# Kernel optimization log

Measured on AMD Instinct MI355X. Metric: run time of the kernel, lower is better.

Reference implementation:

```python
import jax, jax.numpy as jnp
import numpy as np


def setup_inputs() -> dict:
    key = jax.random.key(0)
    k1, k2, k3 = jax.random.split(key, 3)
    N, D, E = 16384, 4096, 64
    x = jax.random.normal(k1, (N, D), dtype=jnp.float32)
    W = jax.random.normal(k2, (E, D), dtype=jnp.float32) * (1.0 / np.sqrt(D))
    b = jax.random.normal(k3, (E,), dtype=jnp.float32) * 0.01
    return {"x": x, "W": W, "b": b, "top_k": 2}


def reference(x, W, b, top_k):
    # logits: [N, E]
    logits = jnp.einsum('nd,ed->ne', x, W) + b
    top_vals, top_idx = jax.lax.top_k(logits, top_k)          # [N, k]
    top_probs = jax.nn.softmax(top_vals, axis=-1)             # softmax over the k selected logits
    N = logits.shape[0]
    rows = jnp.arange(N)[:, None]                             # [N, 1]
    gates = jnp.zeros_like(logits).at[rows, top_idx].set(top_probs)  # sparse gate tensor [N, E]
    return gates, top_idx
```

## Files before the change

### kernel.cpp

```cpp
#include <hip/hip_runtime.h>
#include <math.h>

typedef _Float16 f16;
typedef _Float16 f16x8 __attribute__((ext_vector_type(8)));
typedef _Float16 f16x4 __attribute__((ext_vector_type(4)));
typedef float    f32x4 __attribute__((ext_vector_type(4)));

constexpr int D_DIM = 4096;
constexpr int E_DIM = 64;
constexpr int BM    = 64;
constexpr int BK    = 64;
constexpr int NT    = 256;
constexpr int LDT   = BK + 8;
constexpr int LDL   = E_DIM + 1;

constexpr float XSCALE  = 8.0f;
constexpr float WSCALE  = 256.0f;
constexpr float UNSCALE = 1.0f / 2048.0f;

__global__ __launch_bounds__(NT) void pack_w(const float* __restrict__ W,
                                             f16* __restrict__ whi,
                                             f16* __restrict__ wlo) {
    const int i = (blockIdx.x * NT + threadIdx.x) * 4;
    const float4 w = *(const float4*)(W + i);
    const float v[4] = {w.x * WSCALE, w.y * WSCALE, w.z * WSCALE, w.w * WSCALE};
    f16x4 hv, lv;
#pragma unroll
    for (int j = 0; j < 4; ++j) {
        const f16 h = (f16)v[j];
        hv[j] = h;
        lv[j] = (f16)(v[j] - (float)h);
    }
    *(f16x4*)(whi + i) = hv;
    *(f16x4*)(wlo + i) = lv;
}

__global__ __launch_bounds__(NT, 4) void gemm_partial(
    const float* __restrict__ x, const f16* __restrict__ whi,
    const f16* __restrict__ wlo, float* __restrict__ partials, int ksplit)
{
    __shared__ alignas(16) f16 Wh[E_DIM * LDT];
    __shared__ alignas(16) f16 Wl[E_DIM * LDT];

    const int tid   = threadIdx.x;
    const int bx    = blockIdx.x;
    const int tile  = bx / ksplit;
    const int split = bx % ksplit;
    const int row0  = tile * BM;
    const int dk    = D_DIM / ksplit;
    const int koff  = split * dk;
    const int KT    = dk / BK;

    const int ks2 = tid & 3;
    const int we  = tid >> 2;

    const int lane = tid & 63;
    const int wv   = tid >> 6;
    const int r0   = wv * 16;
    const int m    = lane & 15;
    const int quad = lane >> 4;

    f32x4 acc[4] = {{0,0,0,0},{0,0,0,0},{0,0,0,0},{0,0,0,0}};

    f16x8 whr[2], wlr[2];
    auto loadW = [&](int t) {
        const size_t o = (size_t)we * D_DIM + koff + t * BK + ks2 * 16;
        whr[0] = *(const f16x8*)(whi + o);
        whr[1] = *(const f16x8*)(whi + o + 8);
        wlr[0] = *(const f16x8*)(wlo + o);
        wlr[1] = *(const f16x8*)(wlo + o + 8);
    };
    auto storeW = [&]() {
        *(f16x8*)&Wh[we * LDT + ks2 * 16]     = whr[0];
        *(f16x8*)&Wh[we * LDT + ks2 * 16 + 8] = whr[1];
        *(f16x8*)&Wl[we * LDT + ks2 * 16]     = wlr[0];
        *(f16x8*)&Wl[we * LDT + ks2 * 16 + 8] = wlr[1];
    };

    const float* xrow = x + (size_t)(row0 + r0 + m) * D_DIM + koff + quad * 8;

    float4 xc[2][2], xn[2][2];
    auto loadX = [&](float4 d[2][2], int t) {
#pragma unroll
        for (int kk = 0; kk < 2; ++kk) {
            const float* p = xrow + t * BK + kk * 32;
            d[kk][0] = ((const float4*)p)[0];
            d[kk][1] = ((const float4*)p)[1];
        }
    };

    loadW(0);
    loadX(xc, 0);
    storeW();
    __syncthreads();

    for (int t = 0; t < KT; ++t) {
        if (t + 1 < KT) { loadW(t + 1); loadX(xn, t + 1); }

#pragma unroll
        for (int kk = 0; kk < 2; ++kk) {
            const float v[8] = {xc[kk][0].x * XSCALE, xc[kk][0].y * XSCALE,
                                xc[kk][0].z * XSCALE, xc[kk][0].w * XSCALE,
                                xc[kk][1].x * XSCALE, xc[kk][1].y * XSCALE,
                                xc[kk][1].z * XSCALE, xc[kk][1].w * XSCALE};
            f16x8 ah, al;
#pragma unroll
            for (int j = 0; j < 8; ++j) {
                const f16 h = (f16)v[j];
                ah[j] = h;
                al[j] = (f16)(v[j] - (float)h);
            }
            const int ko = kk * 32 + quad * 8;
#pragma unroll
            for (int ct = 0; ct < 4; ++ct) {
                const f16x8 bh = *(const f16x8*)&Wh[(ct * 16 + m) * LDT + ko];
                const f16x8 bl = *(const f16x8*)&Wl[(ct * 16 + m) * LDT + ko];
                acc[ct] = __builtin_amdgcn_mfma_f32_16x16x32_f16(ah, bh, acc[ct], 0, 0, 0);
                acc[ct] = __builtin_amdgcn_mfma_f32_16x16x32_f16(al, bh, acc[ct], 0, 0, 0);
                acc[ct] = __builtin_amdgcn_mfma_f32_16x16x32_f16(ah, bl, acc[ct], 0, 0, 0);
            }
        }
        __syncthreads();
        if (t + 1 < KT) {
            storeW();
#pragma unroll
            for (int kk = 0; kk < 2; ++kk) { xc[kk][0] = xn[kk][0]; xc[kk][1] = xn[kk][1]; }
        }
        __syncthreads();
    }

    float* my = partials + (size_t)bx * (BM * E_DIM);
#pragma unroll
    for (int ct = 0; ct < 4; ++ct)
#pragma unroll
        for (int reg = 0; reg < 4; ++reg)
            my[(r0 + quad * 4 + reg) * E_DIM + ct * 16 + m] = acc[ct][reg] * UNSCALE;
}

__global__ __launch_bounds__(NT) void topk_finish_kernel(
    const float* __restrict__ partials, const float* __restrict__ b,
    float* __restrict__ out, int ksplit, int N)
{
    __shared__ float smem[BM * LDL + 256];
    float* Ls  = smem;
    float* aux = smem + BM * LDL;

    const int tid  = threadIdx.x;
    const int tile = blockIdx.x;
    const int row0 = tile * BM;
    const float* base = partials + (size_t)tile * ksplit * (BM * E_DIM);

#pragma unroll
    for (int p = 0; p < 4; ++p) {
        const int f4 = p * 256 + tid;
        const int r  = f4 >> 4;
        const int c4 = f4 & 15;
        float4 s = *(const float4*)(base + (size_t)f4 * 4);
        for (int sp = 1; sp < ksplit; ++sp) {
            const float4 t4 = *(const float4*)(base + (size_t)sp * (BM * E_DIM) + (size_t)f4 * 4);
            s.x += t4.x; s.y += t4.y; s.z += t4.z; s.w += t4.w;
        }
        const float4 bb = ((const float4*)b)[c4];
        Ls[r * LDL + c4 * 4 + 0] = s.x + bb.x;
        Ls[r * LDL + c4 * 4 + 1] = s.y + bb.y;
        Ls[r * LDL + c4 * 4 + 2] = s.z + bb.z;
        Ls[r * LDL + c4 * 4 + 3] = s.w + bb.w;
    }
    __syncthreads();

    if (tid < BM) {
        const float* lr = &Ls[tid * LDL];
        float v1 = -INFINITY, v2 = -INFINITY;
        int i1 = 0, i2 = 0;
        for (int e = 0; e < E_DIM; ++e) {
            const float v = lr[e];
            if (v > v1)      { v2 = v1; i2 = i1; v1 = v; i1 = e; }
            else if (v > v2) { v2 = v;  i2 = e; }
        }
        const float ex = expf(v2 - v1);
        const float dn = 1.0f + ex;
        aux[tid]       = (float)i1;
        aux[64 + tid]  = (float)i2;
        aux[128 + tid] = 1.0f / dn;
        aux[192 + tid] = ex / dn;
        const size_t basei = (size_t)N * E_DIM + (size_t)(row0 + tid) * 2;
        out[basei]     = (float)i1;
        out[basei + 1] = (float)i2;
    }
    __syncthreads();

#pragma unroll
    for (int p = 0; p < 4; ++p) {
        const int f4 = p * 256 + tid;
        const int r  = f4 >> 4;
        const int c4 = f4 & 15;
        const int i1 = (int)aux[r];
        const int i2 = (int)aux[64 + r];
        const float p1 = aux[128 + r];
        const float p2 = aux[192 + r];
        const int e = c4 * 4;
        float4 g;
        g.x = (e + 0 == i1) ? p1 : (e + 0 == i2) ? p2 : 0.0f;
        g.y = (e + 1 == i1) ? p1 : (e + 1 == i2) ? p2 : 0.0f;
        g.z = (e + 2 == i1) ? p1 : (e + 2 == i2) ? p2 : 0.0f;
        g.w = (e + 3 == i1) ? p1 : (e + 3 == i2) ? p2 : 0.0f;
        *(float4*)(out + (size_t)(row0 + r) * E_DIM + e) = g;
    }
}

extern "C" void kernel_launch(void* const* d_in, const int* in_sizes, int n_in,
                              void* d_out, int out_size, void* d_ws, size_t ws_size,
                              hipStream_t stream) {
    const float* x = (const float*)d_in[0];
    const float* W = (const float*)d_in[1];
    const float* b = (const float*)d_in[2];
    float* out = (float*)d_out;
    const int N = in_sizes[0] / D_DIM;
    const int ntiles = N / BM;

    f16* whi = (f16*)d_ws;
    f16* wlo = whi + (size_t)E_DIM * D_DIM;
    float* partials = (float*)(wlo + (size_t)E_DIM * D_DIM);

    const size_t wplanes = 2 * (size_t)E_DIM * D_DIM * sizeof(f16);
    const size_t pbytes  = (size_t)BM * E_DIM * sizeof(float);
    int ksplit = 1;
    if      (ws_size >= wplanes + (size_t)ntiles * 4 * pbytes) ksplit = 4;
    else if (ws_size >= wplanes + (size_t)ntiles * 2 * pbytes) ksplit = 2;

    hipLaunchKernelGGL(pack_w, dim3((E_DIM * D_DIM) / (NT * 4)), dim3(NT),
                       0, stream, W, whi, wlo);
    hipLaunchKernelGGL(gemm_partial, dim3(ntiles * ksplit), dim3(NT),
                       0, stream, x, whi, wlo, partials, ksplit);
    hipLaunchKernelGGL(topk_finish_kernel, dim3(ntiles), dim3(NT),
                       0, stream, partials, b, out, ksplit, N);
}
```

Measured before the change: 392.1 us.

## Fuse gating GEMM with top-k finish using in-block K split

Merges the partial GEMM and the top-k/softmax finish kernel into one kernel. Each block now handles 32 rows, and its four waves split the K dimension into two halves, which are reduced through shared memory before the top-k. This removes the global partials buffer round trip and one kernel launch. The cost is that each block now stages both W halves into shared memory, raising LDS use and halving the rows that share each W tile load, so W traffic per row doubles.

```diff
diff --git a/kernel.cpp b/kernel.cpp
--- a/kernel.cpp
+++ b/kernel.cpp
@@ -6,13 +6,16 @@
 typedef _Float16 f16x4 __attribute__((ext_vector_type(4)));
 typedef float    f32x4 __attribute__((ext_vector_type(4)));
 
-constexpr int D_DIM = 4096;
-constexpr int E_DIM = 64;
-constexpr int BM    = 64;
-constexpr int BK    = 64;
-constexpr int NT    = 256;
-constexpr int LDT   = BK + 8;
-constexpr int LDL   = E_DIM + 1;
+constexpr int D_DIM   = 4096;
+constexpr int E_DIM   = 64;
+constexpr int BM      = 32;
+constexpr int BK      = 64;
+constexpr int NT      = 256;
+constexpr int KHALVES = 2;
+constexpr int DK      = D_DIM / KHALVES;
+constexpr int KT      = DK / BK;
+constexpr int LDT     = BK + 8;
+constexpr int LDL     = E_DIM + 1;
 
 constexpr float XSCALE  = 8.0f;
 constexpr float WSCALE  = 256.0f;
@@ -35,46 +38,52 @@
     *(f16x4*)(wlo + i) = lv;
 }
 
-__global__ __launch_bounds__(NT, 4) void gemm_partial(
+__global__ __launch_bounds__(NT, 2) void moe_gate_fused(
     const float* __restrict__ x, const f16* __restrict__ whi,
-    const f16* __restrict__ wlo, float* __restrict__ partials, int ksplit)
+    const f16* __restrict__ wlo, const float* __restrict__ b,
+    float* __restrict__ out, int N)
 {
-    __shared__ alignas(16) f16 Wh[E_DIM * LDT];
-    __shared__ alignas(16) f16 Wl[E_DIM * LDT];
-
-    const int tid   = threadIdx.x;
-    const int bx    = blockIdx.x;
-    const int tile  = bx / ksplit;
-    const int split = bx % ksplit;
-    const int row0  = tile * BM;
-    const int dk    = D_DIM / ksplit;
-    const int koff  = split * dk;
-    const int KT    = dk / BK;
+    __shared__ alignas(16) f16 Wh[KHALVES][E_DIM * LDT];
+    __shared__ alignas(16) f16 Wl[KHALVES][E_DIM * LDT];
+    __shared__ float Ls[BM * LDL];
+    __shared__ float aux[4 * BM];
+
+    const int tid  = threadIdx.x;
+    const int row0 = blockIdx.x * BM;
 
     const int ks2 = tid & 3;
     const int we  = tid >> 2;
 
     const int lane = tid & 63;
     const int wv   = tid >> 6;
-    const int r0   = wv * 16;
+    const int half = wv >> 1;
+    const int rg   = wv & 1;
+    const int r0   = rg * 16;
     const int m    = lane & 15;
     const int quad = lane >> 4;
+    const int koff = half * DK;
 
     f32x4 acc[4] = {{0,0,0,0},{0,0,0,0},{0,0,0,0},{0,0,0,0}};
 
-    f16x8 whr[2], wlr[2];
+    f16x8 whr[KHALVES][2], wlr[KHALVES][2];
     auto loadW = [&](int t) {
-        const size_t o = (size_t)we * D_DIM + koff + t * BK + ks2 * 16;
-        whr[0] = *(const f16x8*)(whi + o);
-        whr[1] = *(const f16x8*)(whi + o + 8);
-        wlr[0] = *(const f16x8*)(wlo + o);
-        wlr[1] = *(const f16x8*)(wlo + o + 8);
+#pragma unroll
+        for (int h = 0; h < KHALVES; ++h) {
+            const size_t o = (size_t)we * D_DIM + h * DK + t * BK + ks2 * 16;
+            whr[h][0] = *(const f16x8*)(whi + o);
+            whr[h][1] = *(const f16x8*)(whi + o + 8);
+            wlr[h][0] = *(const f16x8*)(wlo + o);
+            wlr[h][1] = *(const f16x8*)(wlo + o + 8);
+        }
     };
     auto storeW = [&]() {
-        *(f16x8*)&Wh[we * LDT + ks2 * 16]     = whr[0];
-        *(f16x8*)&Wh[we * LDT + ks2 * 16 + 8] = whr[1];
-        *(f16x8*)&Wl[we * LDT + ks2 * 16]     = wlr[0];
-        *(f16x8*)&Wl[we * LDT + ks2 * 16 + 8] = wlr[1];
+#pragma unroll
+        for (int h = 0; h < KHALVES; ++h) {
+            *(f16x8*)&Wh[h][we * LDT + ks2 * 16]     = whr[h][0];
+            *(f16x8*)&Wh[h][we * LDT + ks2 * 16 + 8] = whr[h][1];
+            *(f16x8*)&Wl[h][we * LDT + ks2 * 16]     = wlr[h][0];
+            *(f16x8*)&Wl[h][we * LDT + ks2 * 16 + 8] = wlr[h][1];
+        }
     };
 
     const float* xrow = x + (size_t)(row0 + r0 + m) * D_DIM + koff + quad * 8;
@@ -113,8 +122,8 @@
             const int ko = kk * 32 + quad * 8;
 #pragma unroll
             for (int ct = 0; ct < 4; ++ct) {
-                const f16x8 bh = *(const f16x8*)&Wh[(ct * 16 + m) * LDT + ko];
-                const f16x8 bl = *(const f16x8*)&Wl[(ct * 16 + m) * LDT + ko];
+                const f16x8 bh = *(const f16x8*)&Wh[half][(ct * 16 + m) * LDT + ko];
+                const f16x8 bl = *(const f16x8*)&Wl[half][(ct * 16 + m) * LDT + ko];
                 acc[ct] = __builtin_amdgcn_mfma_f32_16x16x32_f16(ah, bh, acc[ct], 0, 0, 0);
                 acc[ct] = __builtin_amdgcn_mfma_f32_16x16x32_f16(al, bh, acc[ct], 0, 0, 0);
                 acc[ct] = __builtin_amdgcn_mfma_f32_16x16x32_f16(ah, bl, acc[ct], 0, 0, 0);
@@ -129,42 +138,23 @@
         __syncthreads();
     }
 
-    float* my = partials + (size_t)bx * (BM * E_DIM);
-#pragma unroll
-    for (int ct = 0; ct < 4; ++ct)
-#pragma unroll
-        for (int reg = 0; reg < 4; ++reg)
-            my[(r0 + quad * 4 + reg) * E_DIM + ct * 16 + m] = acc[ct][reg] * UNSCALE;
-}
-
-__global__ __launch_bounds__(NT) void topk_finish_kernel(
-    const float* __restrict__ partials, const float* __restrict__ b,
-    float* __restrict__ out, int ksplit, int N)
-{
-    __shared__ float smem[BM * LDL + 256];
-    float* Ls  = smem;
-    float* aux = smem + BM * LDL;
-
-    const int tid  = threadIdx.x;
-    const int tile = blockIdx.x;
-    const int row0 = tile * BM;
-    const float* base = partials + (size_t)tile * ksplit * (BM * E_DIM);
-
-#pragma unroll
-    for (int p = 0; p < 4; ++p) {
-        const int f4 = p * 256 + tid;
-        const int r  = f4 >> 4;
-        const int c4 = f4 & 15;
-        float4 s = *(const float4*)(base + (size_t)f4 * 4);
-        for (int sp = 1; sp < ksplit; ++sp) {
-            const float4 t4 = *(const float4*)(base + (size_t)sp * (BM * E_DIM) + (size_t)f4 * 4);
-            s.x += t4.x; s.y += t4.y; s.z += t4.z; s.w += t4.w;
-        }
-        const float4 bb = ((const float4*)b)[c4];
-        Ls[r * LDL + c4 * 4 + 0] = s.x + bb.x;
-        Ls[r * LDL + c4 * 4 + 1] = s.y + bb.y;
-        Ls[r * LDL + c4 * 4 + 2] = s.z + bb.z;
-        Ls[r * LDL + c4 * 4 + 3] = s.w + bb.w;
+    if (half == 1) {
+#pragma unroll
+        for (int ct = 0; ct < 4; ++ct)
+#pragma unroll
+            for (int reg = 0; reg < 4; ++reg)
+                Ls[(r0 + quad * 4 + reg) * LDL + ct * 16 + m] = acc[ct][reg];
+    }
+    __syncthreads();
+    if (half == 0) {
+#pragma unroll
+        for (int ct = 0; ct < 4; ++ct)
+#pragma unroll
+            for (int reg = 0; reg < 4; ++reg) {
+                const int r = r0 + quad * 4 + reg;
+                const int e = ct * 16 + m;
+                Ls[r * LDL + e] = (acc[ct][reg] + Ls[r * LDL + e]) * UNSCALE + b[e];
+            }
     }
     __syncthreads();
 
@@ -179,10 +169,10 @@
         }
         const float ex = expf(v2 - v1);
         const float dn = 1.0f + ex;
-        aux[tid]       = (float)i1;
-        aux[64 + tid]  = (float)i2;
-        aux[128 + tid] = 1.0f / dn;
-        aux[192 + tid] = ex / dn;
+        aux[tid]          = (float)i1;
+        aux[BM + tid]     = (float)i2;
+        aux[2 * BM + tid] = 1.0f / dn;
+        aux[3 * BM + tid] = ex / dn;
         const size_t basei = (size_t)N * E_DIM + (size_t)(row0 + tid) * 2;
         out[basei]     = (float)i1;
         out[basei + 1] = (float)i2;
@@ -190,14 +180,14 @@
     __syncthreads();
 
 #pragma unroll
-    for (int p = 0; p < 4; ++p) {
-        const int f4 = p * 256 + tid;
+    for (int p = 0; p < 2; ++p) {
+        const int f4 = p * NT + tid;
         const int r  = f4 >> 4;
         const int c4 = f4 & 15;
         const int i1 = (int)aux[r];
-        const int i2 = (int)aux[64 + r];
-        const float p1 = aux[128 + r];
-        const float p2 = aux[192 + r];
+        const int i2 = (int)aux[BM + r];
+        const float p1 = aux[2 * BM + r];
+        const float p2 = aux[3 * BM + r];
         const int e = c4 * 4;
         float4 g;
         g.x = (e + 0 == i1) ? p1 : (e + 0 == i2) ? p2 : 0.0f;
@@ -220,18 +210,9 @@
 
     f16* whi = (f16*)d_ws;
     f16* wlo = whi + (size_t)E_DIM * D_DIM;
-    float* partials = (float*)(wlo + (size_t)E_DIM * D_DIM);
-
-    const size_t wplanes = 2 * (size_t)E_DIM * D_DIM * sizeof(f16);
-    const size_t pbytes  = (size_t)BM * E_DIM * sizeof(float);
-    int ksplit = 1;
-    if      (ws_size >= wplanes + (size_t)ntiles * 4 * pbytes) ksplit = 4;
-    else if (ws_size >= wplanes + (size_t)ntiles * 2 * pbytes) ksplit = 2;
 
     hipLaunchKernelGGL(pack_w, dim3((E_DIM * D_DIM) / (NT * 4)), dim3(NT),
                        0, stream, W, whi, wlo);
-    hipLaunchKernelGGL(gemm_partial, dim3(ntiles * ksplit), dim3(NT),
-                       0, stream, x, whi, wlo, partials, ksplit);
-    hipLaunchKernelGGL(topk_finish_kernel, dim3(ntiles), dim3(NT),
-                       0, stream, partials, b, out, ksplit, N);
+    hipLaunchKernelGGL(moe_gate_fused, dim3(ntiles), dim3(NT),
+                       0, stream, x, whi, wlo, b, out, N);
 }
```

New measurement: 380.0 us. -3.1%, faster.
